# Kernel optimization log

Measured on AMD Instinct MI355X. Metric: run time of the kernel, lower is better.

The kernel has to match this reference:

```python
import jax, jax.numpy as jnp
import numpy as np

# ---- config (matches init_kwargs) ----
M, N, D = 8, 512, 243            # meshes, neurons per mesh, input dim
E_RATIO = 0.8
NE = int(N * E_RATIO)            # 409 excitatory
NI = N - NE                      # 103 inhibitory
TICKS = 16
BATCH = 512
BITS = 4
WSCALE = 8.0
VTH, VRESET = 1.0, 0.0
TAU_E, TAU_I, DT = 2.0, 1.5, 1.0
BETA = 10.0                      # fast-sigmoid surrogate slope
INPUT_SCALE = 1.0


def fake_quant(w):
    """Quantization-aware fake quant with straight-through estimator."""
    step = WSCALE / (2 ** (BITS - 1))          # 1.0 for 4-bit, scale 8
    q = jnp.clip(jnp.round(w / step), -(2 ** (BITS - 1)), 2 ** (BITS - 1) - 1) * step
    return w + jax.lax.stop_gradient(q - w)


@jax.custom_vjp
def spike(u):
    return (u >= 0.0).astype(u.dtype)

def _spike_fwd(u):
    return spike(u), u

def _spike_bwd(u, g):
    # fast-sigmoid surrogate gradient
    return (g * BETA / (1.0 + BETA * jnp.abs(u)) ** 2,)

spike.defvjp(_spike_fwd, _spike_bwd)


def setup_inputs() -> dict:
    key = jax.random.key(0)
    ks = jax.random.split(key, 8)

    def sparse_w(k, shape, density, std, zero_diag=False):
        km, kw = jax.random.split(k)
        mask = (jax.random.uniform(km, shape) < density).astype(jnp.float32)
        if zero_diag:
            mask = mask * (1.0 - jnp.eye(shape[-1], dtype=jnp.float32))
        return jax.random.normal(kw, shape) * std * mask

    x = jax.random.normal(ks[0], (BATCH, D), dtype=jnp.float32)
    W_in = jax.random.normal(ks[1], (M, N, D)) * 0.8      # per-mesh input projection [out,in]
    b_in = jax.random.normal(ks[2], (M, N)) * 0.05
    W_inter = sparse_w(ks[3], (M, N, NE), 0.3, 0.8)        # inter-mesh: E of mesh m -> mesh m+1
    W_EE = sparse_w(ks[4], (M, NE, NE), 0.5, 0.8, True)
    W_EI = sparse_w(ks[5], (M, NI, NE), 0.6, 0.8)
    W_IE = sparse_w(ks[6], (M, NE, NI), 0.8, 0.8)
    W_II = sparse_w(ks[7], (M, NI, NI), 0.7, 0.8, True)
    return dict(x=x, W_in=W_in, b_in=b_in, W_inter=W_inter,
                W_EE=W_EE, W_EI=W_EI, W_IE=W_IE, W_II=W_II)


def reference(x, W_in, b_in, W_inter, W_EE, W_EI, W_IE, W_II):
    B = x.shape[0]
    decay_E = 1.0 - DT / TAU_E
    decay_I = 1.0 - DT / TAU_I

    # quantize weights once (constant across ticks)
    qW_in, qW_inter = fake_quant(W_in), fake_quant(W_inter)
    qW_EE, qW_EI = fake_quant(W_EE), fake_quant(W_EI)
    qW_IE, qW_II = fake_quant(W_IE), fake_quant(W_II)

    # external input projection, same every tick: [M, B, N]
    ext_proj = jnp.einsum('bd,mnd->mbn', x * INPUT_SCALE, qW_in) + b_in[:, None, :]

    def tick(carry, _):
        e, i, vE, vI, acc = carry          # e:[M,B,NE] i:[M,B,NI]
        # inter-mesh: mesh m receives inter_connections[m-1](e_prev[m-1])
        inter = jnp.einsum('mbe,mne->mbn', e, qW_inter)
        ext = ext_proj + jnp.roll(inter, 1, axis=0)
        cE = ext[:, :, :NE] \
            + jnp.einsum('mbe,mfe->mbf', e, qW_EE) \
            + jnp.einsum('mbi,mfi->mbf', i, qW_IE)
        cI = ext[:, :, NE:] \
            + jnp.einsum('mbe,mfe->mbf', e, qW_EI) \
            + jnp.einsum('mbi,mfi->mbf', i, qW_II)
        # LIF: leaky decay + input, threshold, hard reset
        vE = vE * decay_E + cE * DT
        vI = vI * decay_I + cI * DT
        sE = spike(vE - VTH)
        sI = spike(vI - VTH)
        vE = sE * VRESET + (1.0 - sE) * vE
        vI = sI * VRESET + (1.0 - sI) * vI
        acc = acc + jnp.concatenate([sE, sI], axis=-1)
        return (sE, sI, vE, vI, acc), None

    z = jnp.zeros
    carry0 = (z((M, B, NE)), z((M, B, NI)), z((M, B, NE)), z((M, B, NI)), z((M, B, N)))
    (eF, iF, vEF, vIF, acc), _ = jax.lax.scan(tick, carry0, None, length=TICKS)
    # accumulator laid out mesh-major: [B, M*N]
    return jnp.transpose(acc, (1, 0, 2)).reshape(B, M * N)
```

## Files before the change

### kernel.cpp

```cpp
#include <hip/hip_runtime.h>
#include <hip/hip_bf16.h>

#define Mm 8
#define Nn 512
#define NEe 409
#define NIi 103
#define Bb 512
#define Dd 243
#define Tt 16
#define SPROW 640
#define WCROW 1152
#define DEC_I 0.33333334f
#define NBLK 512
#define FLAGSTRIDE 16
#define SPINMAX 1000000L

typedef int v4i __attribute__((ext_vector_type(4)));
union LV { long l[2]; v4i v; };

__device__ __forceinline__ float quantf(float w) {
    float q = rintf(w);
    return fminf(fmaxf(q, -8.0f), 7.0f);
}

__global__ void k_zero(int* __restrict__ p, int n) {
    int i = blockIdx.x * blockDim.x + threadIdx.x;
    if (i < n) __hip_atomic_store(&p[i], 0, __ATOMIC_RELAXED, __HIP_MEMORY_SCOPE_AGENT);
}

__global__ void k_pack(const float* __restrict__ Wint, const float* __restrict__ WEE,
                       const float* __restrict__ WEI, const float* __restrict__ WIE,
                       const float* __restrict__ WII, signed char* __restrict__ Wc) {
    int i = blockIdx.x * 256 + threadIdx.x;
    if (i >= Mm * Nn * WCROW) return;
    int k = i % WCROW;
    int n = (i / WCROW) & (Nn - 1);
    int m = i / (WCROW * Nn);
    float w = 0.0f;
    if (k < 512) {
        if (k < NEe) w = Wint[((((m + 7) & 7) * Nn) + n) * NEe + k];
    } else if (k < 1024) {
        int j = k - 512;
        if (j < NEe) w = (n < NEe) ? WEE[((m * NEe) + n) * NEe + j]
                                   : WEI[((m * NIi) + (n - NEe)) * NEe + j];
    } else {
        int j = k - 1024;
        if (j < NIi) w = (n < NEe) ? WIE[((m * NEe) + n) * NIi + j]
                                   : WII[((m * NIi) + (n - NEe)) * NIi + j];
    }
    Wc[i] = (signed char)(int)quantf(w);
}

__global__ void k_ext(const float* __restrict__ x, const float* __restrict__ Win,
                      const float* __restrict__ bin, float* __restrict__ ext) {
    __shared__ float xs[64][68];
    __shared__ float wsm[64][68];
    const int bid = blockIdx.x;
    const int m  = bid >> 6;
    const int bt = (bid >> 3) & 7;
    const int nt = bid & 7;
    const int b0 = bt * 64, n0 = nt * 64;
    const int t = threadIdx.x;
    const int tb4 = (t & 15) * 4;
    const int tn4 = (t >> 4) * 4;
    const int sr = t >> 2;
    const int sc = (t & 3) * 16;
    float c[4][4];
#pragma unroll
    for (int i = 0; i < 4; ++i)
#pragma unroll
        for (int j = 0; j < 4; ++j) c[i][j] = 0.0f;

    for (int d0 = 0; d0 < Dd; d0 += 64) {
#pragma unroll
        for (int j = 0; j < 16; ++j) {
            int d = d0 + sc + j;
            float xv = 0.0f, wv = 0.0f;
            if (d < Dd) {
                xv = x[(b0 + sr) * Dd + d];
                wv = quantf(Win[((m * Nn) + n0 + sr) * Dd + d]);
            }
            xs[sc + j][sr] = xv;
            wsm[sc + j][sr] = wv;
        }
        __syncthreads();
        const int dmax = min(64, Dd - d0);
        for (int d = 0; d < dmax; ++d) {
            float4 av = *(const float4*)&xs[d][tb4];
            float4 wv = *(const float4*)&wsm[d][tn4];
            float a[4] = {av.x, av.y, av.z, av.w};
            float wq[4] = {wv.x, wv.y, wv.z, wv.w};
#pragma unroll
            for (int i = 0; i < 4; ++i)
#pragma unroll
                for (int j = 0; j < 4; ++j)
                    c[i][j] = fmaf(a[i], wq[j], c[i][j]);
        }
        __syncthreads();
    }
#pragma unroll
    for (int i = 0; i < 4; ++i)
#pragma unroll
        for (int j = 0; j < 4; ++j) {
            float val = __fadd_rn(c[i][j], bin[m * Nn + n0 + tn4 + j]);
            ext[(size_t)(m * Bb + b0 + tb4 + i) * Nn + n0 + tn4 + j] = val;
        }
}

__device__ __forceinline__ void gbar(int* __restrict__ flags, int* __restrict__ rel,
                                     int t, int wg, int tid) {
    __syncthreads();
    if (tid == 0)
        __hip_atomic_store(&flags[wg * FLAGSTRIDE], t + 1,
                           __ATOMIC_RELAXED, __HIP_MEMORY_SCOPE_AGENT);
    if (wg == 0) {
        long spin = 0;
        while (__hip_atomic_load(&flags[tid * FLAGSTRIDE],
                                 __ATOMIC_RELAXED, __HIP_MEMORY_SCOPE_AGENT) < t + 1) {
            __builtin_amdgcn_s_sleep(2);
            if (++spin > SPINMAX) break;
        }
        spin = 0;
        while (__hip_atomic_load(&flags[(tid + 256) * FLAGSTRIDE],
                                 __ATOMIC_RELAXED, __HIP_MEMORY_SCOPE_AGENT) < t + 1) {
            __builtin_amdgcn_s_sleep(2);
            if (++spin > SPINMAX) break;
        }
        __syncthreads();
        if (tid == 0)
            __hip_atomic_store(rel, t + 1, __ATOMIC_RELAXED, __HIP_MEMORY_SCOPE_AGENT);
    } else if (tid == 0) {
        long spin = 0;
        while (__hip_atomic_load(rel, __ATOMIC_RELAXED, __HIP_MEMORY_SCOPE_AGENT) < t + 1) {
            __builtin_amdgcn_s_sleep(8);
            if (++spin > SPINMAX) break;
        }
    }
    __syncthreads();
}

__global__ void __launch_bounds__(256, 2)
k_ticks(const signed char* __restrict__ Wc,
        signed char* __restrict__ Sp0,
        signed char* __restrict__ Sp1,
        const float* __restrict__ ext,
        float* __restrict__ out,
        int* __restrict__ flags,
        int* __restrict__ rel) {
    __shared__ __align__(16) signed char sA[2][64][128];
    __shared__ __align__(16) signed char sB[2][64][128];

    const int wg = blockIdx.x;
    const int m  = wg & 7;
    const int bt = (wg >> 3) & 7;
    const int nt = wg >> 6;
    const int b0 = bt * 64;
    const int n0 = nt * 64;
    const int pm = (m + 7) & 7;

    const int tid  = threadIdx.x;
    const int w    = tid >> 6;
    const int lane = tid & 63;
    const int bh   = w & 1;
    const int nh   = w >> 1;
    const int quad = lane >> 4;
    const int li   = lane & 15;
    const int lx   = li & 7;

    int rowS[2], gcolS[2], scolS[2];
#pragma unroll
    for (int j = 0; j < 2; ++j) {
        int ch = tid + j * 256;
        rowS[j]  = ch >> 3;
        int cnk  = ch & 7;
        gcolS[j] = cnk * 16;
        scolS[j] = (cnk ^ (rowS[j] & 7)) * 16;
    }

    float decs[2]; int offs[2]; int nels[2];
#pragma unroll
    for (int tn = 0; tn < 2; ++tn) {
        int n = n0 + nh * 32 + tn * 16 + li;
        nels[tn] = n;
        decs[tn] = (n < NEe) ? 0.5f : DEC_I;
        offs[tn] = (n < NEe) ? n : (n + 103);
    }
    const int bbase = b0 + bh * 32;

    const signed char* WcBase = Wc + (size_t)(m * Nn + n0) * WCROW;

    float extr[2][2][4];
#pragma unroll
    for (int tb = 0; tb < 2; ++tb)
#pragma unroll
        for (int tn = 0; tn < 2; ++tn)
#pragma unroll
            for (int r = 0; r < 4; ++r) {
                int b = bbase + tb * 16 + quad * 4 + r;
                extr[tb][tn][r] = ext[(size_t)(m * Bb + b) * Nn + nels[tn]];
            }
    float vmem[2][2][4];
    int cnt[2][2];
#pragma unroll
    for (int tb = 0; tb < 2; ++tb)
#pragma unroll
        for (int tn = 0; tn < 2; ++tn) {
            cnt[tb][tn] = 0;
#pragma unroll
            for (int r = 0; r < 4; ++r) vmem[tb][tn][r] = 0.0f;
        }

    for (int t = 0; t < Tt; ++t) {
        signed char* SR = (t & 1) ? Sp1 : Sp0;
        signed char* SW = (t & 1) ? Sp0 : Sp1;
        signed char* AbasePrev = SR + (size_t)(pm * Bb + b0) * SPROW;
        signed char* AbaseOwn  = SR + (size_t)(m  * Bb + b0) * SPROW;

        v4i acc[2][2];
#pragma unroll
        for (int tb = 0; tb < 2; ++tb)
#pragma unroll
            for (int tn = 0; tn < 2; ++tn) acc[tb][tn] = (v4i){0, 0, 0, 0};
        float c[2][2][4];

#pragma unroll
        for (int j = 0; j < 2; ++j) {
            long* ap = (long*)(AbasePrev + (size_t)rowS[j] * SPROW + gcolS[j]);
            LV tmp;
            tmp.l[0] = __hip_atomic_load(ap,     __ATOMIC_RELAXED, __HIP_MEMORY_SCOPE_AGENT);
            tmp.l[1] = __hip_atomic_load(ap + 1, __ATOMIC_RELAXED, __HIP_MEMORY_SCOPE_AGENT);
            *(v4i*)&sA[0][rowS[j]][scolS[j]] = tmp.v;
            *(v4i*)&sB[0][rowS[j]][scolS[j]] =
                *(const v4i*)(WcBase + (size_t)rowS[j] * WCROW + gcolS[j]);
        }
        __syncthreads();

        for (int it = 0; it < 9; ++it) {
            const int buf = it & 1;
            v4i nA[2], nB[2];
            if (it < 8) {
                const int k0 = (it + 1) * 128;
                signed char* ab; int ko;
                if (k0 < 512) { ab = AbasePrev; ko = k0; }
                else          { ab = AbaseOwn;  ko = k0 - 512; }
#pragma unroll
                for (int j = 0; j < 2; ++j) {
                    long* ap = (long*)(ab + (size_t)rowS[j] * SPROW + ko + gcolS[j]);
                    LV tmp;
                    tmp.l[0] = __hip_atomic_load(ap,     __ATOMIC_RELAXED, __HIP_MEMORY_SCOPE_AGENT);
                    tmp.l[1] = __hip_atomic_load(ap + 1, __ATOMIC_RELAXED, __HIP_MEMORY_SCOPE_AGENT);
                    nA[j] = tmp.v;
                    nB[j] = *(const v4i*)(WcBase + (size_t)rowS[j] * WCROW + k0 + gcolS[j]);
                }
            }
#pragma unroll
            for (int ks = 0; ks < 128; ks += 64) {
                const int c0 = (((ks >> 4) + quad) ^ lx) * 16;
                v4i af0 = *(const v4i*)&sA[buf][bh * 32 + li][c0];
                v4i af1 = *(const v4i*)&sA[buf][bh * 32 + 16 + li][c0];
#pragma unroll
                for (int tn = 0; tn < 2; ++tn) {
                    v4i bfr = *(const v4i*)&sB[buf][nh * 32 + tn * 16 + li][c0];
                    acc[0][tn] = __builtin_amdgcn_mfma_i32_16x16x64_i8(af0, bfr, acc[0][tn], 0, 0, 0);
                    acc[1][tn] = __builtin_amdgcn_mfma_i32_16x16x64_i8(af1, bfr, acc[1][tn], 0, 0, 0);
                }
            }
            if (it < 8) {
                const int nb = buf ^ 1;
#pragma unroll
                for (int j = 0; j < 2; ++j) {
                    *(v4i*)&sA[nb][rowS[j]][scolS[j]] = nA[j];
                    *(v4i*)&sB[nb][rowS[j]][scolS[j]] = nB[j];
                }
            }
            __syncthreads();
            if (it == 3) {
#pragma unroll
                for (int tb = 0; tb < 2; ++tb)
#pragma unroll
                    for (int tn = 0; tn < 2; ++tn) {
#pragma unroll
                        for (int r = 0; r < 4; ++r)
                            c[tb][tn][r] = __fadd_rn(extr[tb][tn][r], (float)acc[tb][tn][r]);
                        acc[tb][tn] = (v4i){0, 0, 0, 0};
                    }
            } else if (it == 7 || it == 8) {
#pragma unroll
                for (int tb = 0; tb < 2; ++tb)
#pragma unroll
                    for (int tn = 0; tn < 2; ++tn) {
#pragma unroll
                        for (int r = 0; r < 4; ++r)
                            c[tb][tn][r] = __fadd_rn(c[tb][tn][r], (float)acc[tb][tn][r]);
                        acc[tb][tn] = (v4i){0, 0, 0, 0};
                    }
            }
        }

#pragma unroll
        for (int tb = 0; tb < 2; ++tb)
#pragma unroll
            for (int tn = 0; tn < 2; ++tn)
#pragma unroll
                for (int r = 0; r < 4; ++r) {
                    float vn = __fadd_rn(__fmul_rn(vmem[tb][tn][r], decs[tn]), c[tb][tn][r]);
                    int s = (vn >= 1.0f) ? 1 : 0;
                    vmem[tb][tn][r] = s ? 0.0f : vn;
                    cnt[tb][tn] += s << (r * 8);
                    if (t < Tt - 1) {
                        int b = bbase + tb * 16 + quad * 4 + r;
                        signed char* sp = SW + (size_t)(m * Bb + b) * SPROW + offs[tn];
                        __hip_atomic_store(sp, (signed char)s,
                                           __ATOMIC_RELAXED, __HIP_MEMORY_SCOPE_AGENT);
                    }
                }
        if (t < Tt - 1) gbar(flags, rel, t, wg, tid);
    }

#pragma unroll
    for (int tb = 0; tb < 2; ++tb)
#pragma unroll
        for (int tn = 0; tn < 2; ++tn)
#pragma unroll
            for (int r = 0; r < 4; ++r) {
                int b = bbase + tb * 16 + quad * 4 + r;
                out[(size_t)b * (Mm * Nn) + m * Nn + nels[tn]] =
                    (float)((cnt[tb][tn] >> (r * 8)) & 0xff);
            }
}

extern "C" void kernel_launch(void* const* d_in, const int* in_sizes, int n_in,
                              void* d_out, int out_size, void* d_ws, size_t ws_size,
                              hipStream_t stream) {
    const float* x    = (const float*)d_in[0];
    const float* Win  = (const float*)d_in[1];
    const float* bin  = (const float*)d_in[2];
    const float* Wint = (const float*)d_in[3];
    const float* WEE  = (const float*)d_in[4];
    const float* WEI  = (const float*)d_in[5];
    const float* WIE  = (const float*)d_in[6];
    const float* WII  = (const float*)d_in[7];
    float* out = (float*)d_out;

    char* ws = (char*)d_ws;
    signed char* Wc  = (signed char*)ws;
    signed char* Sp0 = (signed char*)(ws + 4718592);
    signed char* Sp1 = Sp0 + 2621440;
    int* flags = (int*)(ws + 4718592 + 2 * 2621440);
    int* rel   = (int*)(ws + 4718592 + 2 * 2621440 + 32768);
    float* extw = (float*)(ws + 4718592 + 2 * 2621440 + 32768 + 64);

    int nz = (2 * 2621440 + 32768 + 64) / 4;
    k_zero<<<(nz + 255) / 256, 256, 0, stream>>>((int*)Sp0, nz);
    k_pack<<<(Mm * Nn * WCROW + 255) / 256, 256, 0, stream>>>(Wint, WEE, WEI, WIE, WII, Wc);
    k_ext<<<512, 256, 0, stream>>>(x, Win, bin, extw);

    k_ticks<<<NBLK, 256, 0, stream>>>(Wc, Sp0, Sp1, (const float*)extw, out, flags, rel);
}
```

Before: 244.1 us.

## Fuse input projection into tick kernel, drop zero kernel, skip first-tick matmul

Measured after the change: 258.4 us. +5.9%, slower.

```diff
diff --git a/kernel.cpp b/kernel.cpp
--- a/kernel.cpp
+++ b/kernel.cpp
@@ -21,11 +21,6 @@
 __device__ __forceinline__ float quantf(float w) {
     float q = rintf(w);
     return fminf(fmaxf(q, -8.0f), 7.0f);
-}
-
-__global__ void k_zero(int* __restrict__ p, int n) {
-    int i = blockIdx.x * blockDim.x + threadIdx.x;
-    if (i < n) __hip_atomic_store(&p[i], 0, __ATOMIC_RELAXED, __HIP_MEMORY_SCOPE_AGENT);
 }
 
 __global__ void k_pack(const float* __restrict__ Wint, const float* __restrict__ WEE,
@@ -51,62 +46,6 @@
     Wc[i] = (signed char)(int)quantf(w);
 }
 
-__global__ void k_ext(const float* __restrict__ x, const float* __restrict__ Win,
-                      const float* __restrict__ bin, float* __restrict__ ext) {
-    __shared__ float xs[64][68];
-    __shared__ float wsm[64][68];
-    const int bid = blockIdx.x;
-    const int m  = bid >> 6;
-    const int bt = (bid >> 3) & 7;
-    const int nt = bid & 7;
-    const int b0 = bt * 64, n0 = nt * 64;
-    const int t = threadIdx.x;
-    const int tb4 = (t & 15) * 4;
-    const int tn4 = (t >> 4) * 4;
-    const int sr = t >> 2;
-    const int sc = (t & 3) * 16;
-    float c[4][4];
-#pragma unroll
-    for (int i = 0; i < 4; ++i)
-#pragma unroll
-        for (int j = 0; j < 4; ++j) c[i][j] = 0.0f;
-
-    for (int d0 = 0; d0 < Dd; d0 += 64) {
-#pragma unroll
-        for (int j = 0; j < 16; ++j) {
-            int d = d0 + sc + j;
-            float xv = 0.0f, wv = 0.0f;
-            if (d < Dd) {
-                xv = x[(b0 + sr) * Dd + d];
-                wv = quantf(Win[((m * Nn) + n0 + sr) * Dd + d]);
-            }
-            xs[sc + j][sr] = xv;
-            wsm[sc + j][sr] = wv;
-        }
-        __syncthreads();
-        const int dmax = min(64, Dd - d0);
-        for (int d = 0; d < dmax; ++d) {
-            float4 av = *(const float4*)&xs[d][tb4];
-            float4 wv = *(const float4*)&wsm[d][tn4];
-            float a[4] = {av.x, av.y, av.z, av.w};
-            float wq[4] = {wv.x, wv.y, wv.z, wv.w};
-#pragma unroll
-            for (int i = 0; i < 4; ++i)
-#pragma unroll
-                for (int j = 0; j < 4; ++j)
-                    c[i][j] = fmaf(a[i], wq[j], c[i][j]);
-        }
-        __syncthreads();
-    }
-#pragma unroll
-    for (int i = 0; i < 4; ++i)
-#pragma unroll
-        for (int j = 0; j < 4; ++j) {
-            float val = __fadd_rn(c[i][j], bin[m * Nn + n0 + tn4 + j]);
-            ext[(size_t)(m * Bb + b0 + tb4 + i) * Nn + n0 + tn4 + j] = val;
-        }
-}
-
 __device__ __forceinline__ void gbar(int* __restrict__ flags, int* __restrict__ rel,
                                      int t, int wg, int tid) {
     __syncthreads();
@@ -143,12 +82,18 @@
 k_ticks(const signed char* __restrict__ Wc,
         signed char* __restrict__ Sp0,
         signed char* __restrict__ Sp1,
-        const float* __restrict__ ext,
+        const float* __restrict__ x,
+        const float* __restrict__ Win,
+        const float* __restrict__ bin,
         float* __restrict__ out,
         int* __restrict__ flags,
         int* __restrict__ rel) {
-    __shared__ __align__(16) signed char sA[2][64][128];
-    __shared__ __align__(16) signed char sB[2][64][128];
+    __shared__ __align__(16) char smem[34816];
+    float (*xs)[68]  = (float (*)[68])smem;
+    float (*wsm)[68] = (float (*)[68])(smem + 8704);
+    float (*et)[68]  = (float (*)[68])(smem + 17408);
+    signed char (*sA)[64][128] = (signed char (*)[64][128])smem;
+    signed char (*sB)[64][128] = (signed char (*)[64][128])(smem + 16384);
 
     const int wg = blockIdx.x;
     const int m  = wg & 7;
@@ -190,15 +135,60 @@
     const signed char* WcBase = Wc + (size_t)(m * Nn + n0) * WCROW;
 
     float extr[2][2][4];
-#pragma unroll
-    for (int tb = 0; tb < 2; ++tb)
-#pragma unroll
-        for (int tn = 0; tn < 2; ++tn)
-#pragma unroll
-            for (int r = 0; r < 4; ++r) {
-                int b = bbase + tb * 16 + quad * 4 + r;
-                extr[tb][tn][r] = ext[(size_t)(m * Bb + b) * Nn + nels[tn]];
-            }
+    {
+        const int tb4 = (tid & 15) * 4;
+        const int tn4 = (tid >> 4) * 4;
+        const int sr  = tid >> 2;
+        const int sc  = (tid & 3) * 8;
+        float c4[4][4];
+#pragma unroll
+        for (int i = 0; i < 4; ++i)
+#pragma unroll
+            for (int j = 0; j < 4; ++j) c4[i][j] = 0.0f;
+
+        for (int d0 = 0; d0 < Dd; d0 += 32) {
+#pragma unroll
+            for (int j = 0; j < 8; ++j) {
+                int d = d0 + sc + j;
+                float xv = 0.0f, wv = 0.0f;
+                if (d < Dd) {
+                    xv = x[(b0 + sr) * Dd + d];
+                    wv = quantf(Win[((m * Nn) + n0 + sr) * Dd + d]);
+                }
+                xs[sc + j][sr] = xv;
+                wsm[sc + j][sr] = wv;
+            }
+            __syncthreads();
+            const int dmax = min(32, Dd - d0);
+            for (int d = 0; d < dmax; ++d) {
+                float4 av = *(const float4*)&xs[d][tb4];
+                float4 wv = *(const float4*)&wsm[d][tn4];
+                float a[4] = {av.x, av.y, av.z, av.w};
+                float wq[4] = {wv.x, wv.y, wv.z, wv.w};
+#pragma unroll
+                for (int i = 0; i < 4; ++i)
+#pragma unroll
+                    for (int j = 0; j < 4; ++j)
+                        c4[i][j] = fmaf(a[i], wq[j], c4[i][j]);
+            }
+            __syncthreads();
+        }
+#pragma unroll
+        for (int i = 0; i < 4; ++i)
+#pragma unroll
+            for (int j = 0; j < 4; ++j)
+                et[tb4 + i][tn4 + j] = __fadd_rn(c4[i][j], bin[m * Nn + n0 + tn4 + j]);
+        __syncthreads();
+#pragma unroll
+        for (int tb = 0; tb < 2; ++tb)
+#pragma unroll
+            for (int tn = 0; tn < 2; ++tn)
+#pragma unroll
+                for (int r = 0; r < 4; ++r)
+                    extr[tb][tn][r] = et[bh * 32 + tb * 16 + quad * 4 + r][nh * 32 + tn * 16 + li];
+        __syncthreads();
+    }
+
     float vmem[2][2][4];
     int cnt[2][2];
 #pragma unroll
@@ -209,6 +199,17 @@
 #pragma unroll
             for (int r = 0; r < 4; ++r) vmem[tb][tn][r] = 0.0f;
         }
+
+    if (nt == 0) {
+        for (int idx = tid; idx < 64 * 128 * 2; idx += 256) {
+            int bufsel = idx >> 13;
+            int rr = (idx >> 7) & 63;
+            int p  = idx & 127;
+            int off = (p < 103) ? (409 + p) : (615 + (p - 103));
+            signed char* base = (bufsel ? Sp1 : Sp0) + (size_t)(m * Bb + b0 + rr) * SPROW + off;
+            __hip_atomic_store(base, (signed char)0, __ATOMIC_RELAXED, __HIP_MEMORY_SCOPE_AGENT);
+        }
+    }
 
     for (int t = 0; t < Tt; ++t) {
         signed char* SR = (t & 1) ? Sp1 : Sp0;
@@ -216,84 +217,95 @@
         signed char* AbasePrev = SR + (size_t)(pm * Bb + b0) * SPROW;
         signed char* AbaseOwn  = SR + (size_t)(m  * Bb + b0) * SPROW;
 
-        v4i acc[2][2];
-#pragma unroll
-        for (int tb = 0; tb < 2; ++tb)
-#pragma unroll
-            for (int tn = 0; tn < 2; ++tn) acc[tb][tn] = (v4i){0, 0, 0, 0};
         float c[2][2][4];
 
-#pragma unroll
-        for (int j = 0; j < 2; ++j) {
-            long* ap = (long*)(AbasePrev + (size_t)rowS[j] * SPROW + gcolS[j]);
-            LV tmp;
-            tmp.l[0] = __hip_atomic_load(ap,     __ATOMIC_RELAXED, __HIP_MEMORY_SCOPE_AGENT);
-            tmp.l[1] = __hip_atomic_load(ap + 1, __ATOMIC_RELAXED, __HIP_MEMORY_SCOPE_AGENT);
-            *(v4i*)&sA[0][rowS[j]][scolS[j]] = tmp.v;
-            *(v4i*)&sB[0][rowS[j]][scolS[j]] =
-                *(const v4i*)(WcBase + (size_t)rowS[j] * WCROW + gcolS[j]);
-        }
-        __syncthreads();
-
-        for (int it = 0; it < 9; ++it) {
-            const int buf = it & 1;
-            v4i nA[2], nB[2];
-            if (it < 8) {
-                const int k0 = (it + 1) * 128;
-                signed char* ab; int ko;
-                if (k0 < 512) { ab = AbasePrev; ko = k0; }
-                else          { ab = AbaseOwn;  ko = k0 - 512; }
-#pragma unroll
-                for (int j = 0; j < 2; ++j) {
-                    long* ap = (long*)(ab + (size_t)rowS[j] * SPROW + ko + gcolS[j]);
-                    LV tmp;
-                    tmp.l[0] = __hip_atomic_load(ap,     __ATOMIC_RELAXED, __HIP_MEMORY_SCOPE_AGENT);
-                    tmp.l[1] = __hip_atomic_load(ap + 1, __ATOMIC_RELAXED, __HIP_MEMORY_SCOPE_AGENT);
-                    nA[j] = tmp.v;
-                    nB[j] = *(const v4i*)(WcBase + (size_t)rowS[j] * WCROW + k0 + gcolS[j]);
-                }
-            }
-#pragma unroll
-            for (int ks = 0; ks < 128; ks += 64) {
-                const int c0 = (((ks >> 4) + quad) ^ lx) * 16;
-                v4i af0 = *(const v4i*)&sA[buf][bh * 32 + li][c0];
-                v4i af1 = *(const v4i*)&sA[buf][bh * 32 + 16 + li][c0];
-#pragma unroll
-                for (int tn = 0; tn < 2; ++tn) {
-                    v4i bfr = *(const v4i*)&sB[buf][nh * 32 + tn * 16 + li][c0];
-                    acc[0][tn] = __builtin_amdgcn_mfma_i32_16x16x64_i8(af0, bfr, acc[0][tn], 0, 0, 0);
-                    acc[1][tn] = __builtin_amdgcn_mfma_i32_16x16x64_i8(af1, bfr, acc[1][tn], 0, 0, 0);
-                }
-            }
-            if (it < 8) {
-                const int nb = buf ^ 1;
-#pragma unroll
-                for (int j = 0; j < 2; ++j) {
-                    *(v4i*)&sA[nb][rowS[j]][scolS[j]] = nA[j];
-                    *(v4i*)&sB[nb][rowS[j]][scolS[j]] = nB[j];
-                }
+        if (t == 0) {
+#pragma unroll
+            for (int tb = 0; tb < 2; ++tb)
+#pragma unroll
+                for (int tn = 0; tn < 2; ++tn)
+#pragma unroll
+                    for (int r = 0; r < 4; ++r)
+                        c[tb][tn][r] = __fadd_rn(__fadd_rn(__fadd_rn(extr[tb][tn][r], 0.0f), 0.0f), 0.0f);
+        } else {
+            v4i acc[2][2];
+#pragma unroll
+            for (int tb = 0; tb < 2; ++tb)
+#pragma unroll
+                for (int tn = 0; tn < 2; ++tn) acc[tb][tn] = (v4i){0, 0, 0, 0};
+
+#pragma unroll
+            for (int j = 0; j < 2; ++j) {
+                long* ap = (long*)(AbasePrev + (size_t)rowS[j] * SPROW + gcolS[j]);
+                LV tmp;
+                tmp.l[0] = __hip_atomic_load(ap,     __ATOMIC_RELAXED, __HIP_MEMORY_SCOPE_AGENT);
+                tmp.l[1] = __hip_atomic_load(ap + 1, __ATOMIC_RELAXED, __HIP_MEMORY_SCOPE_AGENT);
+                *(v4i*)&sA[0][rowS[j]][scolS[j]] = tmp.v;
+                *(v4i*)&sB[0][rowS[j]][scolS[j]] =
+                    *(const v4i*)(WcBase + (size_t)rowS[j] * WCROW + gcolS[j]);
             }
             __syncthreads();
-            if (it == 3) {
-#pragma unroll
-                for (int tb = 0; tb < 2; ++tb)
+
+            for (int it = 0; it < 9; ++it) {
+                const int buf = it & 1;
+                v4i nA[2], nB[2];
+                if (it < 8) {
+                    const int k0 = (it + 1) * 128;
+                    signed char* ab; int ko;
+                    if (k0 < 512) { ab = AbasePrev; ko = k0; }
+                    else          { ab = AbaseOwn;  ko = k0 - 512; }
+#pragma unroll
+                    for (int j = 0; j < 2; ++j) {
+                        long* ap = (long*)(ab + (size_t)rowS[j] * SPROW + ko + gcolS[j]);
+                        LV tmp;
+                        tmp.l[0] = __hip_atomic_load(ap,     __ATOMIC_RELAXED, __HIP_MEMORY_SCOPE_AGENT);
+                        tmp.l[1] = __hip_atomic_load(ap + 1, __ATOMIC_RELAXED, __HIP_MEMORY_SCOPE_AGENT);
+                        nA[j] = tmp.v;
+                        nB[j] = *(const v4i*)(WcBase + (size_t)rowS[j] * WCROW + k0 + gcolS[j]);
+                    }
+                }
+#pragma unroll
+                for (int ks = 0; ks < 128; ks += 64) {
+                    const int c0 = (((ks >> 4) + quad) ^ lx) * 16;
+                    v4i af0 = *(const v4i*)&sA[buf][bh * 32 + li][c0];
+                    v4i af1 = *(const v4i*)&sA[buf][bh * 32 + 16 + li][c0];
 #pragma unroll
                     for (int tn = 0; tn < 2; ++tn) {
-#pragma unroll
-                        for (int r = 0; r < 4; ++r)
-                            c[tb][tn][r] = __fadd_rn(extr[tb][tn][r], (float)acc[tb][tn][r]);
-                        acc[tb][tn] = (v4i){0, 0, 0, 0};
+                        v4i bfr = *(const v4i*)&sB[buf][nh * 32 + tn * 16 + li][c0];
+                        acc[0][tn] = __builtin_amdgcn_mfma_i32_16x16x64_i8(af0, bfr, acc[0][tn], 0, 0, 0);
+                        acc[1][tn] = __builtin_amdgcn_mfma_i32_16x16x64_i8(af1, bfr, acc[1][tn], 0, 0, 0);
                     }
-            } else if (it == 7 || it == 8) {
-#pragma unroll
-                for (int tb = 0; tb < 2; ++tb)
-#pragma unroll
-                    for (int tn = 0; tn < 2; ++tn) {
-#pragma unroll
-                        for (int r = 0; r < 4; ++r)
-                            c[tb][tn][r] = __fadd_rn(c[tb][tn][r], (float)acc[tb][tn][r]);
-                        acc[tb][tn] = (v4i){0, 0, 0, 0};
+                }
+                if (it < 8) {
+                    const int nb = buf ^ 1;
+#pragma unroll
+                    for (int j = 0; j < 2; ++j) {
+                        *(v4i*)&sA[nb][rowS[j]][scolS[j]] = nA[j];
+                        *(v4i*)&sB[nb][rowS[j]][scolS[j]] = nB[j];
                     }
+                }
+                __syncthreads();
+                if (it == 3) {
+#pragma unroll
+                    for (int tb = 0; tb < 2; ++tb)
+#pragma unroll
+                        for (int tn = 0; tn < 2; ++tn) {
+#pragma unroll
+                            for (int r = 0; r < 4; ++r)
+                                c[tb][tn][r] = __fadd_rn(extr[tb][tn][r], (float)acc[tb][tn][r]);
+                            acc[tb][tn] = (v4i){0, 0, 0, 0};
+                        }
+                } else if (it == 7 || it == 8) {
+#pragma unroll
+                    for (int tb = 0; tb < 2; ++tb)
+#pragma unroll
+                        for (int tn = 0; tn < 2; ++tn) {
+#pragma unroll
+                            for (int r = 0; r < 4; ++r)
+                                c[tb][tn][r] = __fadd_rn(c[tb][tn][r], (float)acc[tb][tn][r]);
+                            acc[tb][tn] = (v4i){0, 0, 0, 0};
+                        }
+                }
             }
         }
 
@@ -348,12 +360,7 @@
     signed char* Sp1 = Sp0 + 2621440;
     int* flags = (int*)(ws + 4718592 + 2 * 2621440);
     int* rel   = (int*)(ws + 4718592 + 2 * 2621440 + 32768);
-    float* extw = (float*)(ws + 4718592 + 2 * 2621440 + 32768 + 64);
-
-    int nz = (2 * 2621440 + 32768 + 64) / 4;
-    k_zero<<<(nz + 255) / 256, 256, 0, stream>>>((int*)Sp0, nz);
+
     k_pack<<<(Mm * Nn * WCROW + 255) / 256, 256, 0, stream>>>(Wint, WEE, WEI, WIE, WII, Wc);
-    k_ext<<<512, 256, 0, stream>>>(x, Win, bin, extw);
-
-    k_ticks<<<NBLK, 256, 0, stream>>>(Wc, Sp0, Sp1, (const float*)extw, out, flags, rel);
-}
+    k_ticks<<<NBLK, 256, 0, stream>>>(Wc, Sp0, Sp1, x, Win, bin, out, flags, rel);
+}
```

## Drop zeroing kernel, skip first-tick GEMM, vectorize weight packing

Applied to the files above, without the earlier changes.

After: 252.8 us. +3.6%, slower.

```diff
diff --git a/kernel.cpp b/kernel.cpp
--- a/kernel.cpp
+++ b/kernel.cpp
@@ -23,32 +23,33 @@
     return fminf(fmaxf(q, -8.0f), 7.0f);
 }
 
-__global__ void k_zero(int* __restrict__ p, int n) {
-    int i = blockIdx.x * blockDim.x + threadIdx.x;
-    if (i < n) __hip_atomic_store(&p[i], 0, __ATOMIC_RELAXED, __HIP_MEMORY_SCOPE_AGENT);
-}
-
 __global__ void k_pack(const float* __restrict__ Wint, const float* __restrict__ WEE,
                        const float* __restrict__ WEI, const float* __restrict__ WIE,
                        const float* __restrict__ WII, signed char* __restrict__ Wc) {
-    int i = blockIdx.x * 256 + threadIdx.x;
-    if (i >= Mm * Nn * WCROW) return;
-    int k = i % WCROW;
-    int n = (i / WCROW) & (Nn - 1);
-    int m = i / (WCROW * Nn);
-    float w = 0.0f;
-    if (k < 512) {
-        if (k < NEe) w = Wint[((((m + 7) & 7) * Nn) + n) * NEe + k];
-    } else if (k < 1024) {
-        int j = k - 512;
-        if (j < NEe) w = (n < NEe) ? WEE[((m * NEe) + n) * NEe + j]
-                                   : WEI[((m * NIi) + (n - NEe)) * NEe + j];
-    } else {
-        int j = k - 1024;
-        if (j < NIi) w = (n < NEe) ? WIE[((m * NEe) + n) * NIi + j]
-                                   : WII[((m * NIi) + (n - NEe)) * NIi + j];
-    }
-    Wc[i] = (signed char)(int)quantf(w);
+    int q = blockIdx.x * 256 + threadIdx.x;
+    if (q >= (Mm * Nn * WCROW) / 4) return;
+    int k0 = (q * 4) % WCROW;
+    int n  = ((q * 4) / WCROW) & (Nn - 1);
+    int m  = (q * 4) / (WCROW * Nn);
+    char out4[4];
+#pragma unroll
+    for (int j = 0; j < 4; ++j) {
+        int k = k0 + j;
+        float w = 0.0f;
+        if (k < 512) {
+            if (k < NEe) w = Wint[((((m + 7) & 7) * Nn) + n) * NEe + k];
+        } else if (k < 1024) {
+            int jj = k - 512;
+            if (jj < NEe) w = (n < NEe) ? WEE[((m * NEe) + n) * NEe + jj]
+                                        : WEI[((m * NIi) + (n - NEe)) * NEe + jj];
+        } else {
+            int jj = k - 1024;
+            if (jj < NIi) w = (n < NEe) ? WIE[((m * NEe) + n) * NIi + jj]
+                                        : WII[((m * NIi) + (n - NEe)) * NIi + jj];
+        }
+        out4[j] = (signed char)(int)quantf(w);
+    }
+    *(int*)&Wc[q * 4] = *(int*)out4;
 }
 
 __global__ void k_ext(const float* __restrict__ x, const float* __restrict__ Win,
@@ -210,90 +211,112 @@
             for (int r = 0; r < 4; ++r) vmem[tb][tn][r] = 0.0f;
         }
 
+    if (nt == 0) {
+        for (int idx = tid; idx < 64 * 128 * 2; idx += 256) {
+            int bufsel = idx >> 13;
+            int rr = (idx >> 7) & 63;
+            int p  = idx & 127;
+            int off = (p < 103) ? (409 + p) : (615 + (p - 103));
+            signed char* base = (bufsel ? Sp1 : Sp0) + (size_t)(m * Bb + b0 + rr) * SPROW + off;
+            __hip_atomic_store(base, (signed char)0, __ATOMIC_RELAXED, __HIP_MEMORY_SCOPE_AGENT);
+        }
+    }
+
     for (int t = 0; t < Tt; ++t) {
         signed char* SR = (t & 1) ? Sp1 : Sp0;
         signed char* SW = (t & 1) ? Sp0 : Sp1;
         signed char* AbasePrev = SR + (size_t)(pm * Bb + b0) * SPROW;
         signed char* AbaseOwn  = SR + (size_t)(m  * Bb + b0) * SPROW;
 
-        v4i acc[2][2];
-#pragma unroll
-        for (int tb = 0; tb < 2; ++tb)
-#pragma unroll
-            for (int tn = 0; tn < 2; ++tn) acc[tb][tn] = (v4i){0, 0, 0, 0};
         float c[2][2][4];
 
-#pragma unroll
-        for (int j = 0; j < 2; ++j) {
-            long* ap = (long*)(AbasePrev + (size_t)rowS[j] * SPROW + gcolS[j]);
-            LV tmp;
-            tmp.l[0] = __hip_atomic_load(ap,     __ATOMIC_RELAXED, __HIP_MEMORY_SCOPE_AGENT);
-            tmp.l[1] = __hip_atomic_load(ap + 1, __ATOMIC_RELAXED, __HIP_MEMORY_SCOPE_AGENT);
-            *(v4i*)&sA[0][rowS[j]][scolS[j]] = tmp.v;
-            *(v4i*)&sB[0][rowS[j]][scolS[j]] =
-                *(const v4i*)(WcBase + (size_t)rowS[j] * WCROW + gcolS[j]);
-        }
-        __syncthreads();
-
-        for (int it = 0; it < 9; ++it) {
-            const int buf = it & 1;
-            v4i nA[2], nB[2];
-            if (it < 8) {
-                const int k0 = (it + 1) * 128;
-                signed char* ab; int ko;
-                if (k0 < 512) { ab = AbasePrev; ko = k0; }
-                else          { ab = AbaseOwn;  ko = k0 - 512; }
-#pragma unroll
-                for (int j = 0; j < 2; ++j) {
-                    long* ap = (long*)(ab + (size_t)rowS[j] * SPROW + ko + gcolS[j]);
-                    LV tmp;
-                    tmp.l[0] = __hip_atomic_load(ap,     __ATOMIC_RELAXED, __HIP_MEMORY_SCOPE_AGENT);
-                    tmp.l[1] = __hip_atomic_load(ap + 1, __ATOMIC_RELAXED, __HIP_MEMORY_SCOPE_AGENT);
-                    nA[j] = tmp.v;
-                    nB[j] = *(const v4i*)(WcBase + (size_t)rowS[j] * WCROW + k0 + gcolS[j]);
-                }
-            }
-#pragma unroll
-            for (int ks = 0; ks < 128; ks += 64) {
-                const int c0 = (((ks >> 4) + quad) ^ lx) * 16;
-                v4i af0 = *(const v4i*)&sA[buf][bh * 32 + li][c0];
-                v4i af1 = *(const v4i*)&sA[buf][bh * 32 + 16 + li][c0];
-#pragma unroll
-                for (int tn = 0; tn < 2; ++tn) {
-                    v4i bfr = *(const v4i*)&sB[buf][nh * 32 + tn * 16 + li][c0];
-                    acc[0][tn] = __builtin_amdgcn_mfma_i32_16x16x64_i8(af0, bfr, acc[0][tn], 0, 0, 0);
-                    acc[1][tn] = __builtin_amdgcn_mfma_i32_16x16x64_i8(af1, bfr, acc[1][tn], 0, 0, 0);
-                }
-            }
-            if (it < 8) {
-                const int nb = buf ^ 1;
-#pragma unroll
-                for (int j = 0; j < 2; ++j) {
-                    *(v4i*)&sA[nb][rowS[j]][scolS[j]] = nA[j];
-                    *(v4i*)&sB[nb][rowS[j]][scolS[j]] = nB[j];
-                }
+        if (t == 0) {
+#pragma unroll
+            for (int tb = 0; tb < 2; ++tb)
+#pragma unroll
+                for (int tn = 0; tn < 2; ++tn)
+#pragma unroll
+                    for (int r = 0; r < 4; ++r)
+                        c[tb][tn][r] = __fadd_rn(__fadd_rn(__fadd_rn(extr[tb][tn][r], 0.0f), 0.0f), 0.0f);
+        } else {
+            v4i acc[2][2];
+#pragma unroll
+            for (int tb = 0; tb < 2; ++tb)
+#pragma unroll
+                for (int tn = 0; tn < 2; ++tn) acc[tb][tn] = (v4i){0, 0, 0, 0};
+
+#pragma unroll
+            for (int j = 0; j < 2; ++j) {
+                long* ap = (long*)(AbasePrev + (size_t)rowS[j] * SPROW + gcolS[j]);
+                LV tmp;
+                tmp.l[0] = __hip_atomic_load(ap,     __ATOMIC_RELAXED, __HIP_MEMORY_SCOPE_AGENT);
+                tmp.l[1] = __hip_atomic_load(ap + 1, __ATOMIC_RELAXED, __HIP_MEMORY_SCOPE_AGENT);
+                *(v4i*)&sA[0][rowS[j]][scolS[j]] = tmp.v;
+                *(v4i*)&sB[0][rowS[j]][scolS[j]] =
+                    *(const v4i*)(WcBase + (size_t)rowS[j] * WCROW + gcolS[j]);
             }
             __syncthreads();
-            if (it == 3) {
-#pragma unroll
-                for (int tb = 0; tb < 2; ++tb)
+
+            for (int it = 0; it < 9; ++it) {
+                const int buf = it & 1;
+                v4i nA[2], nB[2];
+                if (it < 8) {
+                    const int k0 = (it + 1) * 128;
+                    signed char* ab; int ko;
+                    if (k0 < 512) { ab = AbasePrev; ko = k0; }
+                    else          { ab = AbaseOwn;  ko = k0 - 512; }
+#pragma unroll
+                    for (int j = 0; j < 2; ++j) {
+                        long* ap = (long*)(ab + (size_t)rowS[j] * SPROW + ko + gcolS[j]);
+                        LV tmp;
+                        tmp.l[0] = __hip_atomic_load(ap,     __ATOMIC_RELAXED, __HIP_MEMORY_SCOPE_AGENT);
+                        tmp.l[1] = __hip_atomic_load(ap + 1, __ATOMIC_RELAXED, __HIP_MEMORY_SCOPE_AGENT);
+                        nA[j] = tmp.v;
+                        nB[j] = *(const v4i*)(WcBase + (size_t)rowS[j] * WCROW + k0 + gcolS[j]);
+                    }
+                }
+#pragma unroll
+                for (int ks = 0; ks < 128; ks += 64) {
+                    const int c0 = (((ks >> 4) + quad) ^ lx) * 16;
+                    v4i af0 = *(const v4i*)&sA[buf][bh * 32 + li][c0];
+                    v4i af1 = *(const v4i*)&sA[buf][bh * 32 + 16 + li][c0];
 #pragma unroll
                     for (int tn = 0; tn < 2; ++tn) {
-#pragma unroll
-                        for (int r = 0; r < 4; ++r)
-                            c[tb][tn][r] = __fadd_rn(extr[tb][tn][r], (float)acc[tb][tn][r]);
-                        acc[tb][tn] = (v4i){0, 0, 0, 0};
+                        v4i bfr = *(const v4i*)&sB[buf][nh * 32 + tn * 16 + li][c0];
+                        acc[0][tn] = __builtin_amdgcn_mfma_i32_16x16x64_i8(af0, bfr, acc[0][tn], 0, 0, 0);
+                        acc[1][tn] = __builtin_amdgcn_mfma_i32_16x16x64_i8(af1, bfr, acc[1][tn], 0, 0, 0);
                     }
-            } else if (it == 7 || it == 8) {
-#pragma unroll
-                for (int tb = 0; tb < 2; ++tb)
-#pragma unroll
-                    for (int tn = 0; tn < 2; ++tn) {
-#pragma unroll
-                        for (int r = 0; r < 4; ++r)
-                            c[tb][tn][r] = __fadd_rn(c[tb][tn][r], (float)acc[tb][tn][r]);
-                        acc[tb][tn] = (v4i){0, 0, 0, 0};
+                }
+                if (it < 8) {
+                    const int nb = buf ^ 1;
+#pragma unroll
+                    for (int j = 0; j < 2; ++j) {
+                        *(v4i*)&sA[nb][rowS[j]][scolS[j]] = nA[j];
+                        *(v4i*)&sB[nb][rowS[j]][scolS[j]] = nB[j];
                     }
+                }
+                __syncthreads();
+                if (it == 3) {
+#pragma unroll
+                    for (int tb = 0; tb < 2; ++tb)
+#pragma unroll
+                        for (int tn = 0; tn < 2; ++tn) {
+#pragma unroll
+                            for (int r = 0; r < 4; ++r)
+                                c[tb][tn][r] = __fadd_rn(extr[tb][tn][r], (float)acc[tb][tn][r]);
+                            acc[tb][tn] = (v4i){0, 0, 0, 0};
+                        }
+                } else if (it == 7 || it == 8) {
+#pragma unroll
+                    for (int tb = 0; tb < 2; ++tb)
+#pragma unroll
+                        for (int tn = 0; tn < 2; ++tn) {
+#pragma unroll
+                            for (int r = 0; r < 4; ++r)
+                                c[tb][tn][r] = __fadd_rn(c[tb][tn][r], (float)acc[tb][tn][r]);
+                            acc[tb][tn] = (v4i){0, 0, 0, 0};
+                        }
+                }
             }
         }
 
@@ -350,10 +373,7 @@
     int* rel   = (int*)(ws + 4718592 + 2 * 2621440 + 32768);
     float* extw = (float*)(ws + 4718592 + 2 * 2621440 + 32768 + 64);
 
-    int nz = (2 * 2621440 + 32768 + 64) / 4;
-    k_zero<<<(nz + 255) / 256, 256, 0, stream>>>((int*)Sp0, nz);
-    k_pack<<<(Mm * Nn * WCROW + 255) / 256, 256, 0, stream>>>(Wint, WEE, WEI, WIE, WII, Wc);
+    k_pack<<<(Mm * Nn * WCROW / 4 + 255) / 256, 256, 0, stream>>>(Wint, WEE, WEI, WIE, WII, Wc);
     k_ext<<<512, 256, 0, stream>>>(x, Win, bin, extw);
-
     k_ticks<<<NBLK, 256, 0, stream>>>(Wc, Sp0, Sp1, (const float*)extw, out, flags, rel);
 }
```
